# Performance work log

Measured on AMD Instinct MI355X. Metric: run time of the kernel, lower is better.

The kernel has to match this reference:

```python
import jax, jax.numpy as jnp
import numpy as np

L, N, IN, H, NL = 512, 64, 256, 1024, 2


def setup_inputs() -> dict:
    key = jax.random.key(0)
    ks = jax.random.split(key, 11)
    s = 1.0 / np.sqrt(H)  # torch init scale ~ U(-sqrt(1/H), sqrt(1/H))
    return {
        'x': jax.random.normal(ks[0], (L, N, IN), jnp.float32),
        'h0': jax.random.normal(ks[1], (NL, N, H), jnp.float32) * 0.1,
        'c0': jax.random.normal(ks[2], (NL, N, H), jnp.float32) * 0.1,
        'w_ih0': jax.random.normal(ks[3], (4 * H, IN), jnp.float32) * s,
        'w_hh0': jax.random.normal(ks[4], (4 * H, H), jnp.float32) * s,
        'b_ih0': jax.random.normal(ks[5], (4 * H,), jnp.float32) * s,
        'b_hh0': jax.random.normal(ks[6], (4 * H,), jnp.float32) * s,
        'w_ih1': jax.random.normal(ks[7], (4 * H, H), jnp.float32) * s,
        'w_hh1': jax.random.normal(ks[8], (4 * H, H), jnp.float32) * s,
        'b_ih1': jax.random.normal(ks[9], (4 * H,), jnp.float32) * s,
        'b_hh1': jax.random.normal(ks[10], (4 * H,), jnp.float32) * s,
    }


def _lstm_layer(x_seq, h0, c0, w_ih, w_hh, b_ih, b_hh):
    # x_seq: (L, N, D_in); precompute input-side gate activations once (big GEMM)
    gates_x = jnp.einsum('lnd,gd->lng', x_seq, w_ih) + b_ih + b_hh  # (L, N, 4H)

    def step(carry, gx):
        h, c = carry
        gates = gx + h @ w_hh.T  # (N, 4H)
        i, f, g, o = jnp.split(gates, 4, axis=-1)
        c = jax.nn.sigmoid(f) * c + jax.nn.sigmoid(i) * jnp.tanh(g)
        h = jax.nn.sigmoid(o) * jnp.tanh(c)
        return (h, c), (h, c)

    (hT, cT), (hs, cs) = jax.lax.scan(step, (h0, c0), gates_x)
    return hs, cs, hT, cT  # hs,cs: (L, N, H)


def reference(x, h0, c0, w_ih0, w_hh0, b_ih0, b_hh0, w_ih1, w_hh1, b_ih1, b_hh1):
    hs0, cs0, hT0, cT0 = _lstm_layer(x, h0[0], c0[0], w_ih0, w_hh0, b_ih0, b_hh0)
    hs1, cs1, hT1, cT1 = _lstm_layer(hs0, h0[1], c0[1], w_ih1, w_hh1, b_ih1, b_hh1)
    output = hs1                                   # (L, N, H)
    all_c = jnp.stack([cs0, cs1], axis=1)          # (L, num_layers, N, H)
    h_n = jnp.stack([hT0, hT1], axis=0)            # (num_layers, N, H)
    c_n = jnp.stack([cT0, cT1], axis=0)
    return output, all_c, h_n, c_n
```

## Files before the change

### kernel.cpp

```cpp
#include <hip/hip_runtime.h>


typedef unsigned short u16;
typedef unsigned int u32;
typedef __attribute__((ext_vector_type(8))) short short8;
typedef __attribute__((ext_vector_type(4))) float float4v;
typedef __attribute__((ext_vector_type(4))) int int4v;

#define WP0_OFF   0u
#define WP1_OFF   10485760u
#define XB_OFF    27262976u
#define HB0_OFF   44040192u
#define HB1_OFF   44302336u
#define BC0_OFF   44564480u
#define BC1_OFF   44580864u
#define BAR_OFF   44597248u

#define OUT_Y_OFF 0
#define ALLC_OFF  33554432
#define HN_OFF    100663296
#define CN_OFF    100794368

#define SC_BYTE_OFF 131584
#define LDS_BYTES   140032

__device__ inline u16 f2b(float v) {
  union { float f; unsigned u; } a; a.f = v;
  unsigned r = a.u + 0x7FFFu + ((a.u >> 16) & 1u);
  return (u16)(r >> 16);
}

__device__ inline float sigf(float x) { return 1.0f / (1.0f + __expf(-x)); }
__device__ inline float tanh_fast(float x) { return 1.0f - 2.0f / (1.0f + __expf(2.0f * x)); }

__device__ __attribute__((always_inline)) inline short8 ldg_sc(const u16* p) {
  short8 r;
  asm volatile("global_load_dwordx4 %0, %1, off sc0 sc1" : "=v"(r) : "v"(p));
  return r;
}
__device__ __attribute__((always_inline)) inline void stg_sc(u32* p, u32 v) {
  asm volatile("global_store_dword %0, %1, off sc0 sc1" : : "v"(p), "v"(v) : "memory");
}

template<int N>
__device__ __attribute__((always_inline)) inline void wait_vm() {
  static_assert(N % 4 == 0 && N >= 0 && N <= 36, "bad vmcnt");
  if constexpr (N == 0)  asm volatile("s_waitcnt vmcnt(0)" ::: "memory");
  if constexpr (N == 4)  asm volatile("s_waitcnt vmcnt(4)" ::: "memory");
  if constexpr (N == 8)  asm volatile("s_waitcnt vmcnt(8)" ::: "memory");
  if constexpr (N == 12) asm volatile("s_waitcnt vmcnt(12)" ::: "memory");
  if constexpr (N == 16) asm volatile("s_waitcnt vmcnt(16)" ::: "memory");
  if constexpr (N == 20) asm volatile("s_waitcnt vmcnt(20)" ::: "memory");
  if constexpr (N == 24) asm volatile("s_waitcnt vmcnt(24)" ::: "memory");
  if constexpr (N == 28) asm volatile("s_waitcnt vmcnt(28)" ::: "memory");
  if constexpr (N == 32) asm volatile("s_waitcnt vmcnt(32)" ::: "memory");
  if constexpr (N == 36) asm volatile("s_waitcnt vmcnt(36)" ::: "memory");
}


__global__ void pack_w0(const float* __restrict__ w_ih, const float* __restrict__ w_hh,
                        u16* __restrict__ wp) {
  int k = blockIdx.x * 256 + threadIdx.x;
  int q = blockIdx.y;
  int b = blockIdx.z;
  int g = q >> 3, jj = q & 7;
  int r = g * 1024 + b * 8 + jj;
  float v = (k < 256) ? w_ih[r * 256 + k] : w_hh[r * 1024 + (k - 256)];
  wp[(b * 32 + q) * 1280 + k] = f2b(v);
}

__global__ void pack_w1(const float* __restrict__ w_ih, const float* __restrict__ w_hh,
                        u16* __restrict__ wp) {
  int k = blockIdx.x * 256 + threadIdx.x;
  int q = blockIdx.y;
  int b = blockIdx.z;
  int g = q >> 3, jj = q & 7;
  int r = g * 1024 + b * 8 + jj;
  float v = (k < 1024) ? w_ih[r * 1024 + k] : w_hh[r * 1024 + (k - 1024)];
  wp[(b * 32 + q) * 2048 + k] = f2b(v);
}

__global__ void prep_misc(const float* __restrict__ x, const float* __restrict__ h0,
                          const float* __restrict__ bih0, const float* __restrict__ bhh0,
                          const float* __restrict__ bih1, const float* __restrict__ bhh1,
                          u16* __restrict__ xb, u16* __restrict__ hb0, u16* __restrict__ hb1,
                          float* __restrict__ bc0, float* __restrict__ bc1,
                          unsigned* __restrict__ bar) {
  int i = blockIdx.x * 256 + threadIdx.x;
  if (i < 8388608) { xb[i] = f2b(x[i]); return; }
  i -= 8388608;
  if (i < 65536) { hb0[i] = f2b(h0[i]); return; }
  i -= 65536;
  if (i < 65536) { hb1[i] = f2b(h0[65536 + i]); return; }
  i -= 65536;
  if (i < 4096) { bc0[i] = bih0[i] + bhh0[i]; return; }
  i -= 4096;
  if (i < 4096) { bc1[i] = bih1[i] + bhh1[i]; return; }
  i -= 4096;
  if (i < 1024) bar[i] = 0u;
}

__device__ inline void grid_barrier(unsigned* __restrict__ bar, int gi) {
  asm volatile("s_waitcnt vmcnt(0)" ::: "memory");
  __syncthreads();
  if (threadIdx.x == 0) {
    unsigned* gen = bar + 576;
    unsigned g = __hip_atomic_load(gen, __ATOMIC_RELAXED, __HIP_MEMORY_SCOPE_AGENT);
    unsigned a = __hip_atomic_fetch_add(bar + gi * 32, 1u, __ATOMIC_RELAXED, __HIP_MEMORY_SCOPE_AGENT);
    bool flipped = false;
    if ((a & 15u) == 15u) {
      unsigned r = __hip_atomic_fetch_add(bar + 512, 1u, __ATOMIC_RELAXED, __HIP_MEMORY_SCOPE_AGENT);
      if ((r & 15u) == 15u) {
        __hip_atomic_store(gen, g + 1u, __ATOMIC_RELAXED, __HIP_MEMORY_SCOPE_AGENT);
        flipped = true;
      }
    }
    if (!flipped) {
      while (__hip_atomic_load(gen, __ATOMIC_RELAXED, __HIP_MEMORY_SCOPE_AGENT) == g)
        __builtin_amdgcn_s_sleep(2);
    }
  }
  __syncthreads();
  asm volatile("" ::: "memory");
}

template<int KQ, int SW, int PF, int KS>
__device__ __attribute__((always_inline)) inline
void kstep(const u16* __restrict__ pA, const u16* __restrict__ pB,
           const int4v& offA, const int4v& offB, const u16* __restrict__ Wl,
           int brow0, int brow1, int base, short8 (&as)[PF][4], float4v (&acc)[4][2]) {
  if constexpr (KS < KQ) {
    const int gks = base + KS;
    short8 b0 = *(const short8*)&Wl[brow0 + gks * 32];
    short8 b1 = *(const short8*)&Wl[brow1 + gks * 32];
    constexpr int REM = KQ - 1 - KS;
    constexpr int W = 4 * (REM < (PF - 1) ? REM : (PF - 1));
    wait_vm<W>();
    __builtin_amdgcn_sched_barrier(0);
#pragma unroll
    for (int mt = 0; mt < 4; ++mt) {
      acc[mt][0] = __builtin_amdgcn_mfma_f32_16x16x32_bf16(as[KS % PF][mt], b0, acc[mt][0], 0, 0, 0);
      acc[mt][1] = __builtin_amdgcn_mfma_f32_16x16x32_bf16(as[KS % PF][mt], b1, acc[mt][1], 0, 0, 0);
    }
    if constexpr (KS + PF < KQ) {
      const int gn = base + KS + PF;
#pragma unroll
      for (int mt = 0; mt < 4; ++mt) {
        const u16* ap = (gn < SW) ? (pA + offA[mt] + gn * 32)
                                  : (pB + offB[mt] + (gn - SW) * 32);
        as[KS % PF][mt] = ldg_sc(ap);
      }
    }
    kstep<KQ, SW, PF, KS + 1>(pA, pB, offA, offB, Wl, brow0, brow1, base, as, acc);
  }
}

template<int KQ, int SW, int PF>
__device__ __attribute__((always_inline)) inline
void kloop(const u16* __restrict__ pA, const u16* __restrict__ pB,
           const int4v& offA, const int4v& offB, const u16* __restrict__ Wl,
           int brow0, int brow1, int wv, float4v (&acc)[4][2]) {
  static_assert(PF <= KQ, "prefetch depth > trip count");
  const int base = wv * KQ;
  short8 as[PF][4];
#pragma unroll
  for (int p = 0; p < PF; ++p) {
    const int gks = base + p;
#pragma unroll
    for (int mt = 0; mt < 4; ++mt) {
      const u16* ap = (gks < SW) ? (pA + offA[mt] + gks * 32)
                                 : (pB + offB[mt] + (gks - SW) * 32);
      as[p][mt] = ldg_sc(ap);
    }
  }
  kstep<KQ, SW, PF, 0>(pA, pB, offA, offB, Wl, brow0, brow1, base, as, acc);
}

__global__ void __launch_bounds__(256, 1)
lstm_persist(const u16* __restrict__ wp0, const u16* __restrict__ wp1,
             const u16* __restrict__ xb, u16* __restrict__ hb0, u16* __restrict__ hb1,
             const float* __restrict__ bc0, const float* __restrict__ bc1,
             const float* __restrict__ c0in, float* __restrict__ out,
             unsigned* __restrict__ bar) {
  extern __shared__ char smem[];
  u16* Wl = (u16*)smem;
  float* sc = (float*)(smem + SC_BYTE_OFF);

  const int b = blockIdx.x;
  const int layer = b >> 7;
  const int blk = b & 127;
  const int tid = threadIdx.x;
  const int lane = tid & 63;
  const int wv = tid >> 6;
  const int l15 = lane & 15;
  const int qd = lane >> 4;
  const int qd8 = qd * 8;

  const int K = layer ? 2048 : 1280;
  const int KP = K + 8;
  const u16* wsrc = layer ? (wp1 + blk * 32 * 2048) : (wp0 + blk * 32 * 1280);

  for (int q = 0; q < 32; ++q) {
    int k = tid * 8;
    if (k < K) *(short8*)&Wl[q * KP + k] = *(const short8*)&wsrc[q * K + k];
  }
  __syncthreads();

  float* out_y = out + OUT_Y_OFF;
  float* all_c = out + ALLC_OFF;
  float* h_n   = out + HN_OFF;
  float* c_n   = out + CN_OFF;

  const int mrow = wv * 16 + (lane >> 2);
  const int cp2  = (lane & 3) * 2;
  const int col0 = blk * 8 + cp2;
  const float* bcl = layer ? bc1 : bc0;
  const float bi0 = bcl[col0],        bi1 = bcl[col0 + 1];
  const float bf0 = bcl[1024 + col0], bf1 = bcl[1025 + col0];
  const float bg0 = bcl[2048 + col0], bg1 = bcl[2049 + col0];
  const float bo0 = bcl[3072 + col0], bo1 = bcl[3073 + col0];
  float cs0 = c0in[layer * 65536 + mrow * 1024 + col0];
  float cs1 = c0in[layer * 65536 + mrow * 1024 + col0 + 1];

  int4v offA, offB;
#pragma unroll
  for (int mt = 0; mt < 4; ++mt) {
    int row = mt * 16 + l15;
    offA[mt] = layer ? (row * 1024 + qd8) : (row * 256 + qd8);
    offB[mt] = row * 1024 + qd8;
  }
  const int brow0 = l15 * KP + qd8;
  const int brow1 = (16 + l15) * KP + qd8;
  const int gi = b >> 4;

  for (int s = 0; s <= 512; ++s) {
    const bool act = layer ? (s >= 1) : (s < 512);
    const int t = layer ? (s - 1) : s;

    if (act) for (int i = tid; i < 2112; i += 256) sc[i] = 0.0f;
    __syncthreads();

    if (act) {
      const u16* pA; const u16* pB;
      if (layer == 0) { pA = xb + t * 16384;               pB = hb0 + (t & 1) * 65536; }
      else            { pA = hb0 + ((t + 1) & 1) * 65536;  pB = hb1 + (t & 1) * 65536; }

      float4v acc[4][2];
      float4v zz = {0.0f, 0.0f, 0.0f, 0.0f};
#pragma unroll
      for (int mt = 0; mt < 4; ++mt) { acc[mt][0] = zz; acc[mt][1] = zz; }

      if (layer == 0) kloop<10, 8, 10>(pA, pB, offA, offB, Wl, brow0, brow1, wv, acc);
      else            kloop<16, 32, 10>(pA, pB, offA, offB, Wl, brow0, brow1, wv, acc);

#pragma unroll
      for (int mt = 0; mt < 4; ++mt)
#pragma unroll
        for (int nt = 0; nt < 2; ++nt)
#pragma unroll
          for (int r = 0; r < 4; ++r)
            atomicAdd(&sc[(mt * 16 + qd * 4 + r) * 33 + nt * 16 + l15], acc[mt][nt][r]);
    }
    __syncthreads();

    if (act) {
      u16* hnx = (layer ? hb1 : hb0) + ((t + 1) & 1) * 65536;
      const float* srow = sc + mrow * 33;
      float gI0 = srow[cp2]          + bi0;
      float gI1 = srow[cp2 + 1]      + bi1;
      float gF0 = srow[8 + cp2]      + bf0;
      float gF1 = srow[9 + cp2]      + bf1;
      float gG0 = srow[16 + cp2]     + bg0;
      float gG1 = srow[17 + cp2]     + bg1;
      float gO0 = srow[24 + cp2]     + bo0;
      float gO1 = srow[25 + cp2]     + bo1;
      float cn0 = sigf(gF0) * cs0 + sigf(gI0) * tanh_fast(gG0);
      float cn1 = sigf(gF1) * cs1 + sigf(gI1) * tanh_fast(gG1);
      float hn0 = sigf(gO0) * tanh_fast(cn0);
      float hn1 = sigf(gO1) * tanh_fast(cn1);
      cs0 = cn0; cs1 = cn1;

      u32 hv = (u32)f2b(hn0) | ((u32)f2b(hn1) << 16);
      stg_sc((u32*)(hnx + mrow * 1024 + col0), hv);

      const int oidx = mrow * 1024 + col0;
      if (layer == 0) {
        __builtin_nontemporal_store(cn0, &all_c[t * 131072 + oidx]);
        __builtin_nontemporal_store(cn1, &all_c[t * 131072 + oidx + 1]);
      } else {
        __builtin_nontemporal_store(cn0, &all_c[t * 131072 + 65536 + oidx]);
        __builtin_nontemporal_store(cn1, &all_c[t * 131072 + 65536 + oidx + 1]);
        __builtin_nontemporal_store(hn0, &out_y[t * 65536 + oidx]);
        __builtin_nontemporal_store(hn1, &out_y[t * 65536 + oidx + 1]);
      }
      if (t == 511) {
        __builtin_nontemporal_store(hn0, &h_n[layer * 65536 + oidx]);
        __builtin_nontemporal_store(hn1, &h_n[layer * 65536 + oidx + 1]);
        __builtin_nontemporal_store(cn0, &c_n[layer * 65536 + oidx]);
        __builtin_nontemporal_store(cn1, &c_n[layer * 65536 + oidx + 1]);
      }
    }
    grid_barrier(bar, gi);
  }
}

extern "C" void kernel_launch(void* const* d_in, const int* in_sizes, int n_in,
                              void* d_out, int out_size, void* d_ws, size_t ws_size,
                              hipStream_t stream) {
  (void)in_sizes; (void)n_in; (void)out_size; (void)ws_size;
  const float* x     = (const float*)d_in[0];
  const float* h0i   = (const float*)d_in[1];
  const float* c0i   = (const float*)d_in[2];
  const float* w_ih0 = (const float*)d_in[3];
  const float* w_hh0 = (const float*)d_in[4];
  const float* b_ih0 = (const float*)d_in[5];
  const float* b_hh0 = (const float*)d_in[6];
  const float* w_ih1 = (const float*)d_in[7];
  const float* w_hh1 = (const float*)d_in[8];
  const float* b_ih1 = (const float*)d_in[9];
  const float* b_hh1 = (const float*)d_in[10];
  float* out = (float*)d_out;
  char* ws = (char*)d_ws;

  u16* wp0 = (u16*)(ws + WP0_OFF);
  u16* wp1 = (u16*)(ws + WP1_OFF);
  u16* xb  = (u16*)(ws + XB_OFF);
  u16* hb0 = (u16*)(ws + HB0_OFF);
  u16* hb1 = (u16*)(ws + HB1_OFF);
  float* bc0 = (float*)(ws + BC0_OFF);
  float* bc1 = (float*)(ws + BC1_OFF);
  unsigned* bar = (unsigned*)(ws + BAR_OFF);

  pack_w0<<<dim3(5, 32, 128), 256, 0, stream>>>(w_ih0, w_hh0, wp0);
  pack_w1<<<dim3(8, 32, 128), 256, 0, stream>>>(w_ih1, w_hh1, wp1);
  prep_misc<<<33316, 256, 0, stream>>>(x, h0i, b_ih0, b_hh0, b_ih1, b_hh1,
                                       xb, hb0, hb1, bc0, bc1, bar);

  hipFuncSetAttribute((const void*)lstm_persist,
                      hipFuncAttributeMaxDynamicSharedMemorySize, LDS_BYTES);
  lstm_persist<<<256, 256, LDS_BYTES, stream>>>(wp0, wp1, xb, hb0, hb1,
                                                bc0, bc1, c0i, out, bar);
}
```

Before: 10.90 ms.

## Split global barrier into per-layer barriers with decoupled layer-to-layer publish flags

Replaces the single grid-wide barrier that lockstepped both LSTM layers with separate per-layer hierarchical barriers, plus publish counters so layer 1 waits only for layer 0's step t and layer 0 may run up to a few steps ahead using a 4-deep h buffer. This removes cross-layer coupling from every step's sync and lets the two layer pipelines drift. It also specializes the layer via templates, clears the LDS scratch inline, and uses paired nontemporal stores with a partial vmcnt wait. Risks include subtle ordering bugs in the relaxed-atomic flag protocol and ring-buffer reuse.

```diff
diff --git a/kernel.cpp b/kernel.cpp
--- a/kernel.cpp
+++ b/kernel.cpp
@@ -4,6 +4,7 @@
 typedef unsigned short u16;
 typedef unsigned int u32;
 typedef __attribute__((ext_vector_type(8))) short short8;
+typedef __attribute__((ext_vector_type(2))) float float2v;
 typedef __attribute__((ext_vector_type(4))) float float4v;
 typedef __attribute__((ext_vector_type(4))) int int4v;
 
@@ -11,10 +12,10 @@
 #define WP1_OFF   10485760u
 #define XB_OFF    27262976u
 #define HB0_OFF   44040192u
-#define HB1_OFF   44302336u
-#define BC0_OFF   44564480u
-#define BC1_OFF   44580864u
-#define BAR_OFF   44597248u
+#define HB1_OFF   44564480u
+#define BC0_OFF   44826624u
+#define BC1_OFF   44843008u
+#define BAR_OFF   44859392u
 
 #define OUT_Y_OFF 0
 #define ALLC_OFF  33554432
@@ -24,6 +25,15 @@
 #define SC_BYTE_OFF 131584
 #define LDS_BYTES   140032
 
+#define ARR0 0
+#define ARR1 256
+#define L2C0 512
+#define L2C1 544
+#define GEN0 576
+#define GEN1 896
+#define PUB0 1216
+#define PUB1 1536
+
 __device__ inline u16 f2b(float v) {
   union { float f; unsigned u; } a; a.f = v;
   unsigned r = a.u + 0x7FFFu + ((a.u >> 16) & 1u);
@@ -41,11 +51,17 @@
 __device__ __attribute__((always_inline)) inline void stg_sc(u32* p, u32 v) {
   asm volatile("global_store_dword %0, %1, off sc0 sc1" : : "v"(p), "v"(v) : "memory");
 }
+__device__ __attribute__((always_inline)) inline void stg_nt2(float* p, float a, float b) {
+  float2v v; v.x = a; v.y = b;
+  asm volatile("global_store_dwordx2 %0, %1, off nt" : : "v"(p), "v"(v) : "memory");
+}
 
 template<int N>
 __device__ __attribute__((always_inline)) inline void wait_vm() {
-  static_assert(N % 4 == 0 && N >= 0 && N <= 36, "bad vmcnt");
+  static_assert(N >= 0 && N <= 36, "bad vmcnt");
   if constexpr (N == 0)  asm volatile("s_waitcnt vmcnt(0)" ::: "memory");
+  if constexpr (N == 1)  asm volatile("s_waitcnt vmcnt(1)" ::: "memory");
+  if constexpr (N == 2)  asm volatile("s_waitcnt vmcnt(2)" ::: "memory");
   if constexpr (N == 4)  asm volatile("s_waitcnt vmcnt(4)" ::: "memory");
   if constexpr (N == 8)  asm volatile("s_waitcnt vmcnt(8)" ::: "memory");
   if constexpr (N == 12) asm volatile("s_waitcnt vmcnt(12)" ::: "memory");
@@ -89,39 +105,50 @@
   int i = blockIdx.x * 256 + threadIdx.x;
   if (i < 8388608) { xb[i] = f2b(x[i]); return; }
   i -= 8388608;
-  if (i < 65536) { hb0[i] = f2b(h0[i]); return; }
+  if (i < 65536) { hb0[3 * 65536 + i] = f2b(h0[i]); return; }
   i -= 65536;
-  if (i < 65536) { hb1[i] = f2b(h0[65536 + i]); return; }
+  if (i < 65536) { hb1[65536 + i] = f2b(h0[65536 + i]); return; }
   i -= 65536;
   if (i < 4096) { bc0[i] = bih0[i] + bhh0[i]; return; }
   i -= 4096;
   if (i < 4096) { bc1[i] = bih1[i] + bhh1[i]; return; }
   i -= 4096;
-  if (i < 1024) bar[i] = 0u;
-}
-
-__device__ inline void grid_barrier(unsigned* __restrict__ bar, int gi) {
-  asm volatile("s_waitcnt vmcnt(0)" ::: "memory");
+  if (i < 2048) bar[i] = 0u;
+}
+
+__device__ __attribute__((always_inline)) inline
+void layer_barrier(unsigned* __restrict__ bar, int gi, unsigned step,
+                   int arrBase, int l2Idx, int genBase, int pubBase) {
   __syncthreads();
   if (threadIdx.x == 0) {
-    unsigned* gen = bar + 576;
-    unsigned g = __hip_atomic_load(gen, __ATOMIC_RELAXED, __HIP_MEMORY_SCOPE_AGENT);
-    unsigned a = __hip_atomic_fetch_add(bar + gi * 32, 1u, __ATOMIC_RELAXED, __HIP_MEMORY_SCOPE_AGENT);
-    bool flipped = false;
+    unsigned a = __hip_atomic_fetch_add(bar + arrBase + gi * 32, 1u,
+                                        __ATOMIC_RELAXED, __HIP_MEMORY_SCOPE_AGENT);
     if ((a & 15u) == 15u) {
-      unsigned r = __hip_atomic_fetch_add(bar + 512, 1u, __ATOMIC_RELAXED, __HIP_MEMORY_SCOPE_AGENT);
-      if ((r & 15u) == 15u) {
-        __hip_atomic_store(gen, g + 1u, __ATOMIC_RELAXED, __HIP_MEMORY_SCOPE_AGENT);
-        flipped = true;
+      unsigned r = __hip_atomic_fetch_add(bar + l2Idx, 1u,
+                                          __ATOMIC_RELAXED, __HIP_MEMORY_SCOPE_AGENT);
+      if ((r & 7u) == 7u) {
+        unsigned v = step + 1u;
+        for (int g = 0; g < 8; ++g)
+          __hip_atomic_store(bar + genBase + g * 32, v, __ATOMIC_RELAXED, __HIP_MEMORY_SCOPE_AGENT);
+        for (int g = 0; g < 8; ++g)
+          __hip_atomic_store(bar + pubBase + g * 32, v, __ATOMIC_RELAXED, __HIP_MEMORY_SCOPE_AGENT);
       }
     }
-    if (!flipped) {
-      while (__hip_atomic_load(gen, __ATOMIC_RELAXED, __HIP_MEMORY_SCOPE_AGENT) == g)
-        __builtin_amdgcn_s_sleep(2);
-    }
+    while ((int)(__hip_atomic_load(bar + genBase + gi * 32, __ATOMIC_RELAXED,
+                                   __HIP_MEMORY_SCOPE_AGENT) - (step + 1u)) < 0)
+      __builtin_amdgcn_s_sleep(1);
   }
   __syncthreads();
-  asm volatile("" ::: "memory");
+}
+
+__device__ __attribute__((always_inline)) inline
+void wait_pub(unsigned* __restrict__ bar, int idx, unsigned need) {
+  if (threadIdx.x == 0) {
+    while ((int)(__hip_atomic_load(bar + idx, __ATOMIC_RELAXED,
+                                   __HIP_MEMORY_SCOPE_AGENT) - need) < 0)
+      __builtin_amdgcn_s_sleep(1);
+  }
+  __syncthreads();
 }
 
 template<int KQ, int SW, int PF, int KS>
@@ -176,6 +203,125 @@
   kstep<KQ, SW, PF, 0>(pA, pB, offA, offB, Wl, brow0, brow1, base, as, acc);
 }
 
+template<int LAYER>
+__device__ __attribute__((always_inline)) inline
+void run_layer(const u16* __restrict__ wp, const u16* __restrict__ xb,
+               u16* __restrict__ hb0, u16* __restrict__ hb1,
+               const float* __restrict__ bc, const float* __restrict__ c0in,
+               float* __restrict__ out, unsigned* __restrict__ bar,
+               u16* Wl, float* sc, int blk) {
+  constexpr int K   = LAYER ? 2048 : 1280;
+  constexpr int KP  = K + 8;
+  constexpr int KQ  = LAYER ? 16 : 10;
+  constexpr int SW  = LAYER ? 32 : 8;
+  constexpr int OUT = LAYER ? 2 : 1;
+
+  const int tid = threadIdx.x;
+  const int lane = tid & 63;
+  const int wv = tid >> 6;
+  const int l15 = lane & 15;
+  const int qd = lane >> 4;
+  const int qd8 = qd * 8;
+  const int gi = blk >> 4;
+
+  const u16* wsrc = wp + blk * 32 * K;
+  for (int q = 0; q < 32; ++q) {
+    int k = tid * 8;
+    if (k < K) *(short8*)&Wl[q * KP + k] = *(const short8*)&wsrc[q * K + k];
+  }
+  for (int i = tid; i < 2112; i += 256) sc[i] = 0.0f;
+  __syncthreads();
+
+  float* out_y = out + OUT_Y_OFF;
+  float* all_c = out + ALLC_OFF;
+  float* h_n   = out + HN_OFF;
+  float* c_n   = out + CN_OFF;
+
+  const int mrow = wv * 16 + (lane >> 2);
+  const int cp2  = (lane & 3) * 2;
+  const int col0 = blk * 8 + cp2;
+  const float bi0 = bc[col0],        bi1 = bc[col0 + 1];
+  const float bf0 = bc[1024 + col0], bf1 = bc[1025 + col0];
+  const float bg0 = bc[2048 + col0], bg1 = bc[2049 + col0];
+  const float bo0 = bc[3072 + col0], bo1 = bc[3073 + col0];
+  float cs0 = c0in[LAYER * 65536 + mrow * 1024 + col0];
+  float cs1 = c0in[LAYER * 65536 + mrow * 1024 + col0 + 1];
+
+  int4v offA, offB;
+#pragma unroll
+  for (int mt = 0; mt < 4; ++mt) {
+    int row = mt * 16 + l15;
+    offA[mt] = LAYER ? (row * 1024 + qd8) : (row * 256 + qd8);
+    offB[mt] = row * 1024 + qd8;
+  }
+  const int brow0 = l15 * KP + qd8;
+  const int brow1 = (16 + l15) * KP + qd8;
+
+  for (int t = 0; t < 512; ++t) {
+    if constexpr (LAYER == 0) {
+      if (t >= 4) wait_pub(bar, PUB1 + gi * 32, (unsigned)(t - 3));
+    } else {
+      wait_pub(bar, PUB0 + gi * 32, (unsigned)(t + 1));
+    }
+
+    const u16* pA; const u16* pB;
+    if constexpr (LAYER == 0) { pA = xb + t * 16384;              pB = hb0 + ((t + 3) & 3) * 65536; }
+    else                      { pA = hb0 + (t & 3) * 65536;       pB = hb1 + ((t + 1) & 1) * 65536; }
+
+    float4v acc[4][2];
+    float4v zz = {0.0f, 0.0f, 0.0f, 0.0f};
+#pragma unroll
+    for (int mt = 0; mt < 4; ++mt) { acc[mt][0] = zz; acc[mt][1] = zz; }
+
+    kloop<KQ, SW, 10>(pA, pB, offA, offB, Wl, brow0, brow1, wv, acc);
+
+#pragma unroll
+    for (int mt = 0; mt < 4; ++mt)
+#pragma unroll
+      for (int nt = 0; nt < 2; ++nt)
+#pragma unroll
+        for (int r = 0; r < 4; ++r)
+          atomicAdd(&sc[(mt * 16 + qd * 4 + r) * 33 + nt * 16 + l15], acc[mt][nt][r]);
+    __syncthreads();
+
+    float* srw = sc + mrow * 33;
+    float gI0 = srw[cp2]      + bi0;  float gI1 = srw[cp2 + 1]  + bi1;
+    float gF0 = srw[8 + cp2]  + bf0;  float gF1 = srw[9 + cp2]  + bf1;
+    float gG0 = srw[16 + cp2] + bg0;  float gG1 = srw[17 + cp2] + bg1;
+    float gO0 = srw[24 + cp2] + bo0;  float gO1 = srw[25 + cp2] + bo1;
+    srw[cp2] = 0.f; srw[cp2 + 1] = 0.f; srw[8 + cp2] = 0.f; srw[9 + cp2] = 0.f;
+    srw[16 + cp2] = 0.f; srw[17 + cp2] = 0.f; srw[24 + cp2] = 0.f; srw[25 + cp2] = 0.f;
+
+    float cn0 = sigf(gF0) * cs0 + sigf(gI0) * tanh_fast(gG0);
+    float cn1 = sigf(gF1) * cs1 + sigf(gI1) * tanh_fast(gG1);
+    float hn0 = sigf(gO0) * tanh_fast(cn0);
+    float hn1 = sigf(gO1) * tanh_fast(cn1);
+    cs0 = cn0; cs1 = cn1;
+
+    u16* hnx = LAYER ? (hb1 + (t & 1) * 65536) : (hb0 + (t & 3) * 65536);
+    u32 hv = (u32)f2b(hn0) | ((u32)f2b(hn1) << 16);
+    stg_sc((u32*)(hnx + mrow * 1024 + col0), hv);
+
+    const int oidx = mrow * 1024 + col0;
+    if constexpr (LAYER == 0) {
+      stg_nt2(&all_c[t * 131072 + oidx], cn0, cn1);
+    } else {
+      stg_nt2(&all_c[t * 131072 + 65536 + oidx], cn0, cn1);
+      stg_nt2(&out_y[t * 65536 + oidx], hn0, hn1);
+    }
+    if (t == 511) {
+      stg_nt2(&h_n[LAYER * 65536 + oidx], hn0, hn1);
+      stg_nt2(&c_n[LAYER * 65536 + oidx], cn0, cn1);
+      wait_vm<0>();
+    } else {
+      wait_vm<OUT>();
+    }
+
+    if constexpr (LAYER == 0) layer_barrier(bar, gi, (unsigned)t, ARR0, L2C0, GEN0, PUB0);
+    else                      layer_barrier(bar, gi, (unsigned)t, ARR1, L2C1, GEN1, PUB1);
+  }
+}
+
 __global__ void __launch_bounds__(256, 1)
 lstm_persist(const u16* __restrict__ wp0, const u16* __restrict__ wp1,
              const u16* __restrict__ xb, u16* __restrict__ hb0, u16* __restrict__ hb1,
@@ -187,121 +333,9 @@
   float* sc = (float*)(smem + SC_BYTE_OFF);
 
   const int b = blockIdx.x;
-  const int layer = b >> 7;
   const int blk = b & 127;
-  const int tid = threadIdx.x;
-  const int lane = tid & 63;
-  const int wv = tid >> 6;
-  const int l15 = lane & 15;
-  const int qd = lane >> 4;
-  const int qd8 = qd * 8;
-
-  const int K = layer ? 2048 : 1280;
-  const int KP = K + 8;
-  const u16* wsrc = layer ? (wp1 + blk * 32 * 2048) : (wp0 + blk * 32 * 1280);
-
-  for (int q = 0; q < 32; ++q) {
-    int k = tid * 8;
-    if (k < K) *(short8*)&Wl[q * KP + k] = *(const short8*)&wsrc[q * K + k];
-  }
-  __syncthreads();
-
-  float* out_y = out + OUT_Y_OFF;
-  float* all_c = out + ALLC_OFF;
-  float* h_n   = out + HN_OFF;
-  float* c_n   = out + CN_OFF;
-
-  const int mrow = wv * 16 + (lane >> 2);
-  const int cp2  = (lane & 3) * 2;
-  const int col0 = blk * 8 + cp2;
-  const float* bcl = layer ? bc1 : bc0;
-  const float bi0 = bcl[col0],        bi1 = bcl[col0 + 1];
-  const float bf0 = bcl[1024 + col0], bf1 = bcl[1025 + col0];
-  const float bg0 = bcl[2048 + col0], bg1 = bcl[2049 + col0];
-  const float bo0 = bcl[3072 + col0], bo1 = bcl[3073 + col0];
-  float cs0 = c0in[layer * 65536 + mrow * 1024 + col0];
-  float cs1 = c0in[layer * 65536 + mrow * 1024 + col0 + 1];
-
-  int4v offA, offB;
-#pragma unroll
-  for (int mt = 0; mt < 4; ++mt) {
-    int row = mt * 16 + l15;
-    offA[mt] = layer ? (row * 1024 + qd8) : (row * 256 + qd8);
-    offB[mt] = row * 1024 + qd8;
-  }
-  const int brow0 = l15 * KP + qd8;
-  const int brow1 = (16 + l15) * KP + qd8;
-  const int gi = b >> 4;
-
-  for (int s = 0; s <= 512; ++s) {
-    const bool act = layer ? (s >= 1) : (s < 512);
-    const int t = layer ? (s - 1) : s;
-
-    if (act) for (int i = tid; i < 2112; i += 256) sc[i] = 0.0f;
-    __syncthreads();
-
-    if (act) {
-      const u16* pA; const u16* pB;
-      if (layer == 0) { pA = xb + t * 16384;               pB = hb0 + (t & 1) * 65536; }
-      else            { pA = hb0 + ((t + 1) & 1) * 65536;  pB = hb1 + (t & 1) * 65536; }
-
-      float4v acc[4][2];
-      float4v zz = {0.0f, 0.0f, 0.0f, 0.0f};
-#pragma unroll
-      for (int mt = 0; mt < 4; ++mt) { acc[mt][0] = zz; acc[mt][1] = zz; }
-
-      if (layer == 0) kloop<10, 8, 10>(pA, pB, offA, offB, Wl, brow0, brow1, wv, acc);
-      else            kloop<16, 32, 10>(pA, pB, offA, offB, Wl, brow0, brow1, wv, acc);
-
-#pragma unroll
-      for (int mt = 0; mt < 4; ++mt)
-#pragma unroll
-        for (int nt = 0; nt < 2; ++nt)
-#pragma unroll
-          for (int r = 0; r < 4; ++r)
-            atomicAdd(&sc[(mt * 16 + qd * 4 + r) * 33 + nt * 16 + l15], acc[mt][nt][r]);
-    }
-    __syncthreads();
-
-    if (act) {
-      u16* hnx = (layer ? hb1 : hb0) + ((t + 1) & 1) * 65536;
-      const float* srow = sc + mrow * 33;
-      float gI0 = srow[cp2]          + bi0;
-      float gI1 = srow[cp2 + 1]      + bi1;
-      float gF0 = srow[8 + cp2]      + bf0;
-      float gF1 = srow[9 + cp2]      + bf1;
-      float gG0 = srow[16 + cp2]     + bg0;
-      float gG1 = srow[17 + cp2]     + bg1;
-      float gO0 = srow[24 + cp2]     + bo0;
-      float gO1 = srow[25 + cp2]     + bo1;
-      float cn0 = sigf(gF0) * cs0 + sigf(gI0) * tanh_fast(gG0);
-      float cn1 = sigf(gF1) * cs1 + sigf(gI1) * tanh_fast(gG1);
-      float hn0 = sigf(gO0) * tanh_fast(cn0);
-      float hn1 = sigf(gO1) * tanh_fast(cn1);
-      cs0 = cn0; cs1 = cn1;
-
-      u32 hv = (u32)f2b(hn0) | ((u32)f2b(hn1) << 16);
-      stg_sc((u32*)(hnx + mrow * 1024 + col0), hv);
-
-      const int oidx = mrow * 1024 + col0;
-      if (layer == 0) {
-        __builtin_nontemporal_store(cn0, &all_c[t * 131072 + oidx]);
-        __builtin_nontemporal_store(cn1, &all_c[t * 131072 + oidx + 1]);
-      } else {
-        __builtin_nontemporal_store(cn0, &all_c[t * 131072 + 65536 + oidx]);
-        __builtin_nontemporal_store(cn1, &all_c[t * 131072 + 65536 + oidx + 1]);
-        __builtin_nontemporal_store(hn0, &out_y[t * 65536 + oidx]);
-        __builtin_nontemporal_store(hn1, &out_y[t * 65536 + oidx + 1]);
-      }
-      if (t == 511) {
-        __builtin_nontemporal_store(hn0, &h_n[layer * 65536 + oidx]);
-        __builtin_nontemporal_store(hn1, &h_n[layer * 65536 + oidx + 1]);
-        __builtin_nontemporal_store(cn0, &c_n[layer * 65536 + oidx]);
-        __builtin_nontemporal_store(cn1, &c_n[layer * 65536 + oidx + 1]);
-      }
-    }
-    grid_barrier(bar, gi);
-  }
+  if (b < 128) run_layer<0>(wp0, xb, hb0, hb1, bc0, c0in, out, bar, Wl, sc, blk);
+  else         run_layer<1>(wp1, xb, hb0, hb1, bc1, c0in, out, bar, Wl, sc, blk);
 }
 
 extern "C" void kernel_launch(void* const* d_in, const int* in_sizes, int n_in,
@@ -333,7 +367,7 @@
 
   pack_w0<<<dim3(5, 32, 128), 256, 0, stream>>>(w_ih0, w_hh0, wp0);
   pack_w1<<<dim3(8, 32, 128), 256, 0, stream>>>(w_ih1, w_hh1, wp1);
-  prep_misc<<<33316, 256, 0, stream>>>(x, h0i, b_ih0, b_hh0, b_ih1, b_hh1,
+  prep_misc<<<33320, 256, 0, stream>>>(x, h0i, b_ih0, b_hh0, b_ih1, b_hh1,
                                        xb, hb0, hb1, bc0, bc1, bar);
 
   hipFuncSetAttribute((const void*)lstm_persist,
```

After: 10.76 ms. Within noise of the previous version (-1.3%).
